# Performance work log

Measured on AMD Instinct MI355X. Metric: run time of the kernel, lower is better.

The kernel has to match this reference:

```python
import jax, jax.numpy as jnp
import numpy as np

N = 100000      # nodes
E = 1600000     # edges (before self-loops)
IN = 128        # in_channels
H = 8           # heads (layer 0)
C = 8           # hidden_node_channels_per_head
OUT = 64        # out_channels (layer 1, single head, concat=False)
NEG_SLOPE = 0.2 # PyG GATConv LeakyReLU slope


def setup_inputs() -> dict:
    key = jax.random.key(0)
    ks = jax.random.split(key, 10)
    x = jax.random.normal(ks[0], (N, IN), jnp.float32)
    edge_index = jax.random.randint(ks[1], (2, E), 0, N, dtype=jnp.int32)
    s0 = 1.0 / np.sqrt(IN)
    s1 = 1.0 / np.sqrt(H * C)
    return {
        "x": x,
        "edge_index": edge_index,
        "W0": jax.random.normal(ks[2], (IN, H * C), jnp.float32) * s0,
        "att_src0": jax.random.normal(ks[3], (H, C), jnp.float32) * s1,
        "att_dst0": jax.random.normal(ks[4], (H, C), jnp.float32) * s1,
        "b0": jnp.zeros((H * C,), jnp.float32),
        "W1": jax.random.normal(ks[5], (H * C, OUT), jnp.float32) * s1,
        "att_src1": jax.random.normal(ks[6], (1, OUT), jnp.float32) * s1,
        "att_dst1": jax.random.normal(ks[7], (1, OUT), jnp.float32) * s1,
        "b1": jnp.zeros((OUT,), jnp.float32),
    }


def _gat_conv(x, src, dst, W, a_src, a_dst, b, heads, ch, concat):
    # x: [N, F_in]; src/dst: [E'] (self-loops included)
    xW = (x @ W).reshape(N, heads, ch)                     # [N, H, C]
    a_s = jnp.einsum('nhc,hc->nh', xW, a_src)              # [N, H]
    a_d = jnp.einsum('nhc,hc->nh', xW, a_dst)              # [N, H]
    e = jax.nn.leaky_relu(a_s[src] + a_d[dst], NEG_SLOPE)  # [E', H]
    # segment softmax over incoming edges of each dst node
    m = jax.ops.segment_max(e, dst, num_segments=N)        # [N, H]
    ex = jnp.exp(e - m[dst])
    denom = jax.ops.segment_sum(ex, dst, num_segments=N)   # [N, H]
    alpha = ex / denom[dst]                                # [E', H]
    out = jax.ops.segment_sum(alpha[:, :, None] * xW[src], dst, num_segments=N)  # [N, H, C]
    if concat:
        return out.reshape(N, heads * ch) + b
    return out.mean(axis=1) + b


def reference(x, edge_index, W0, att_src0, att_dst0, b0, W1, att_src1, att_dst1, b1):
    src, dst = edge_index[0], edge_index[1]
    loops = jnp.arange(N, dtype=src.dtype)                 # PyG add_self_loops=True
    src = jnp.concatenate([src, loops])
    dst = jnp.concatenate([dst, loops])
    # layer 0: GATConv(IN -> C per head, H heads, concat) ; ELU (dropout = identity at eval)
    h = jax.nn.elu(_gat_conv(x, src, dst, W0, att_src0, att_dst0, b0, H, C, True))
    # layer 1: GATConv(H*C -> OUT, 1 head, concat=False) ; ELU
    out = jax.nn.elu(_gat_conv(h, src, dst, W1, att_src1, att_dst1, b1, 1, OUT, False))
    return out
```

## Files before the change

kernel.cpp:

```cpp
#include <hip/hip_runtime.h>
#include <hip/hip_fp16.h>
#include <math.h>


#define CAPS 16
#define STRIDE 17
#define NBMAX 512
#define LOG2E 1.44269504f

typedef _Float16 h2_t  __attribute__((ext_vector_type(2)));
typedef _Float16 h8_t  __attribute__((ext_vector_type(8)));
typedef float    f4_t  __attribute__((ext_vector_type(4)));
typedef unsigned int u4_t __attribute__((ext_vector_type(4)));

__device__ __forceinline__ float lrelu(float v) { return v >= 0.f ? v : 0.2f * v; }
__device__ __forceinline__ float eluf(float v)  {
    return v > 0.f ? v : __builtin_amdgcn_exp2f(v * LOG2E) - 1.f;
}

#define MIX_LO(acc, pk, w) asm("v_fma_mix_f32 %0, %1, %2, %0 op_sel:[0,0,0] op_sel_hi:[1,0,0]" : "+v"(acc) : "v"(pk), "v"(w))
#define MIX_HI(acc, pk, w) asm("v_fma_mix_f32 %0, %1, %2, %0 op_sel:[1,0,0] op_sel_hi:[1,0,0]" : "+v"(acc) : "v"(pk), "v"(w))

__device__ __forceinline__ void gemm_body(
    int gb, const float* __restrict__ x, int N,
    __half* __restrict__ xw, float* __restrict__ as, float* __restrict__ ad,
    h8_t* Bl)
{
    int wave = threadIdx.x >> 6, lane = threadIdx.x & 63;
    int row0 = gb * 128 + wave * 16;
    if (row0 >= N) return;
    int quad = lane >> 4, c16 = lane & 15;
    int myrow = min(row0 + c16, N - 1);
    const float* xr = x + (size_t)myrow * 128;
    h8_t a[4];
    #pragma unroll
    for (int ks = 0; ks < 4; ks++) {
        int kb = ks * 32 + quad * 8;
        float4 v0 = *(const float4*)(xr + kb);
        float4 v1 = *(const float4*)(xr + kb + 4);
        h8_t av;
        av[0] = (_Float16)v0.x; av[1] = (_Float16)v0.y;
        av[2] = (_Float16)v0.z; av[3] = (_Float16)v0.w;
        av[4] = (_Float16)v1.x; av[5] = (_Float16)v1.y;
        av[6] = (_Float16)v1.z; av[7] = (_Float16)v1.w;
        a[ks] = av;
    }
    int rbase = row0 + quad * 4;
    #pragma unroll
    for (int ct = 0; ct < 5; ct++) {
        f4_t acc = {0.f, 0.f, 0.f, 0.f};
        #pragma unroll
        for (int ks = 0; ks < 4; ks++) {
            h8_t b = Bl[(ct * 4 + ks) * 64 + lane];
            acc = __builtin_amdgcn_mfma_f32_16x16x32_f16(a[ks], b, acc, 0, 0, 0);
        }
        if (ct < 4) {
            int col = ct * 16 + c16;
            #pragma unroll
            for (int r = 0; r < 4; r++) {
                int row = rbase + r;
                if (row < N) xw[(size_t)row * 64 + col] = __float2half(acc[r]);
            }
        } else {
            #pragma unroll
            for (int r = 0; r < 4; r++) {
                int row = rbase + r;
                if (row < N) {
                    float sc = acc[r] * LOG2E;
                    if (c16 < 8) as[(size_t)row * 8 + c16] = sc;
                    else         ad[(size_t)row * 8 + (c16 - 8)] = sc;
                }
            }
        }
    }
}

__global__ __launch_bounds__(512, 4) void kGB(
    const float* __restrict__ x, const float* __restrict__ W0,
    const float* __restrict__ aS0, const float* __restrict__ aD0, int N,
    __half* __restrict__ xw, float* __restrict__ as, float* __restrict__ ad,
    int gemmBlocks,
    const int* __restrict__ src, const int* __restrict__ dst, int E, int perBlock,
    unsigned* __restrict__ bucketBuf, int* __restrict__ gcur, int NB, int cap,
    int binBlocks)
{
    __shared__ __align__(16) char smem[NBMAX * STRIDE * 4 + NBMAX * 4];
    int b = blockIdx.x;
    int T = gemmBlocks + binBlocks;
    int lo = (int)((long long)b * gemmBlocks / T);
    int hi = (int)((long long)(b + 1) * gemmBlocks / T);
    if (hi > lo) {
        h8_t* Bl = (h8_t*)smem;
        for (int g = threadIdx.x; g < 1280; g += 512) {
            int col  = g & 15;
            int quad = (g >> 4) & 3;
            int ks   = (g >> 6) & 3;
            int ct   = g >> 8;
            h8_t av;
            if (ct < 4) {
                #pragma unroll
                for (int j = 0; j < 8; j++) {
                    int k = ks * 32 + quad * 8 + j;
                    av[j] = (_Float16)W0[k * 64 + ct * 16 + col];
                }
            } else {
                int h = col & 7;
                const float* att = (col < 8) ? aS0 : aD0;
                #pragma unroll
                for (int j = 0; j < 8; j++) {
                    int k = ks * 32 + quad * 8 + j;
                    float v = 0.f;
                    #pragma unroll
                    for (int cc = 0; cc < 8; cc++)
                        v += W0[k * 64 + h * 8 + cc] * att[h * 8 + cc];
                    av[j] = (_Float16)v;
                }
            }
            Bl[g] = av;
        }
        __syncthreads();
        gemm_body(lo, x, N, xw, as, ad, Bl);
    } else {
        int pb = b - hi;
        unsigned* stage = (unsigned*)smem;
        int* scnt = (int*)(smem + NBMAX * STRIDE * 4);
        int tid = threadIdx.x;
        for (int i = tid; i < NB; i += 512) scnt[i] = 0;
        __syncthreads();
        int e0 = pb * perBlock, e1 = min(E, e0 + perBlock);
        for (int i = e0 + tid; i < e1; i += 512) {
            int d2 = dst[i], s2 = src[i];
            int bk = d2 >> 8;
            unsigned rec = ((unsigned)(d2 & 255) << 22) | (unsigned)s2;
            int pos = atomicAdd(&scnt[bk], 1);
            if (pos < CAPS) {
                stage[bk * STRIDE + pos] = rec;
            } else {
                int g = atomicAdd(&gcur[bk], 1);
                if (g < cap) bucketBuf[(size_t)bk * cap + g] = rec;
            }
        }
        __syncthreads();
        for (int t = tid; t < NB; t += 512) {
            int n = min(scnt[t], CAPS);
            if (n > 0) {
                int gb2 = atomicAdd(&gcur[t], n);
                unsigned* gp = &bucketBuf[(size_t)t * cap + gb2];
                for (int j = 0; j < n; j++)
                    if (gb2 + j < cap) gp[j] = stage[t * STRIDE + j];
            }
        }
    }
}

__global__ __launch_bounds__(256) void kP2(
    const unsigned* __restrict__ bucketBuf, const int* __restrict__ gcur,
    int NB, int cap, int N, int* __restrict__ row, int* __restrict__ adj)
{
    __shared__ int deg[256];
    __shared__ int curl[256];
    __shared__ int sc[256];
    int b = blockIdx.x, tid = threadIdx.x;
    int lo = b << 8;
    int hi = min(N, lo + 256);
    int cnt = hi - lo;
    int size = min(gcur[b], cap);
    int part = 0;
    for (int i = tid; i < b; i += 256) part += min(gcur[i], cap);
    sc[tid] = part;
    __syncthreads();
    for (int off = 128; off > 0; off >>= 1) {
        if (tid < off) sc[tid] += sc[tid + off];
        __syncthreads();
    }
    int bbase = sc[0];
    __syncthreads();
    deg[tid] = 0;
    __syncthreads();
    const unsigned* buf = bucketBuf + (size_t)b * cap;
    for (int e = tid; e < size; e += 256) atomicAdd(&deg[buf[e] >> 22], 1);
    __syncthreads();
    int d = deg[tid];
    sc[tid] = d;
    __syncthreads();
    for (int off = 1; off < 256; off <<= 1) {
        int xv = (tid >= off) ? sc[tid - off] : 0;
        __syncthreads();
        sc[tid] += xv;
        __syncthreads();
    }
    int o = (tid ? sc[tid - 1] : 0);
    curl[tid] = o;
    if (tid < cnt) row[lo + tid] = bbase + o;
    if (b == NB - 1 && tid == 0) row[N] = bbase + size;
    __syncthreads();
    for (int e = tid; e < size; e += 256) {
        unsigned r = buf[e];
        int l = r >> 22;
        int p = atomicAdd(&curl[l], 1);
        adj[bbase + p] = (int)(r & 0x3FFFFF);
    }
}

__global__ __launch_bounds__(512) void k_agg8(
    const __half* __restrict__ xw, const float* __restrict__ as, const float* __restrict__ ad,
    const int* __restrict__ row, const int* __restrict__ adj,
    const float* __restrict__ bias, int N, __half* __restrict__ hbuf)
{
    int n = (blockIdx.x * 512 + threadIdx.x) >> 4;
    int sub  = threadIdx.x & 15;
    if (n >= N) return;
    int e2 = sub >> 3;
    int hh = sub & 7;
    int rs = row[n], re = row[n + 1];
    const u4_t* xwv = (const u4_t*)xw;
    float adv = ad[(unsigned)n * 8u + hh];
    float shift = lrelu(as[(unsigned)n * 8u + hh] + adv);
    float accv[8];
    #pragma unroll
    for (int k = 0; k < 8; k++) accv[k] = 0.f;
    float dsum = 0.f;

    int j = rs;
    bool vA0 = j + e2 < re,     vB0 = j + 2 + e2 < re;
    int  sA0 = adj[(unsigned)(vA0 ? j + e2 : 0)];
    int  sB0 = adj[(unsigned)(vB0 ? j + 2 + e2 : 0)];
    bool vA1 = j + 4 + e2 < re, vB1 = j + 6 + e2 < re;
    int  sA1 = adj[(unsigned)(vA1 ? j + 4 + e2 : 0)];
    int  sB1 = adj[(unsigned)(vB1 ? j + 6 + e2 : 0)];
    float eA0 = lrelu(as[(unsigned)sA0 * 8u + hh] + adv);
    float eB0 = lrelu(as[(unsigned)sB0 * 8u + hh] + adv);
    u4_t xA0 = xwv[(unsigned)sA0 * 8u + hh];
    u4_t xB0 = xwv[(unsigned)sB0 * 8u + hh];
    float eA1, eB1; u4_t xA1, xB1;

    for (;;) {
        {
            bool vA2 = j + 8 + e2 < re, vB2 = j + 10 + e2 < re;
            int nsA = adj[(unsigned)(vA2 ? j + 8 + e2 : 0)];
            int nsB = adj[(unsigned)(vB2 ? j + 10 + e2 : 0)];
            eA1 = lrelu(as[(unsigned)sA1 * 8u + hh] + adv);
            eB1 = lrelu(as[(unsigned)sB1 * 8u + hh] + adv);
            xA1 = xwv[(unsigned)sA1 * 8u + hh];
            xB1 = xwv[(unsigned)sB1 * 8u + hh];
            float wA = vA0 ? __builtin_amdgcn_exp2f(eA0 - shift) : 0.f;
            float wB = vB0 ? __builtin_amdgcn_exp2f(eB0 - shift) : 0.f;
            dsum += wA + wB;
            #pragma unroll
            for (int q = 0; q < 4; q++) {
                MIX_LO(accv[2 * q],     xA0[q], wA);
                MIX_HI(accv[2 * q + 1], xA0[q], wA);
            }
            #pragma unroll
            for (int q = 0; q < 4; q++) {
                MIX_LO(accv[2 * q],     xB0[q], wB);
                MIX_HI(accv[2 * q + 1], xB0[q], wB);
            }
            vA0 = vA2; vB0 = vB2; sA0 = nsA; sB0 = nsB;
        }
        j += 4;
        if (!__any(vA1)) break;
        {
            bool vA2 = j + 8 + e2 < re, vB2 = j + 10 + e2 < re;
            int nsA = adj[(unsigned)(vA2 ? j + 8 + e2 : 0)];
            int nsB = adj[(unsigned)(vB2 ? j + 10 + e2 : 0)];
            eA0 = lrelu(as[(unsigned)sA0 * 8u + hh] + adv);
            eB0 = lrelu(as[(unsigned)sB0 * 8u + hh] + adv);
            xA0 = xwv[(unsigned)sA0 * 8u + hh];
            xB0 = xwv[(unsigned)sB0 * 8u + hh];
            float wA = vA1 ? __builtin_amdgcn_exp2f(eA1 - shift) : 0.f;
            float wB = vB1 ? __builtin_amdgcn_exp2f(eB1 - shift) : 0.f;
            dsum += wA + wB;
            #pragma unroll
            for (int q = 0; q < 4; q++) {
                MIX_LO(accv[2 * q],     xA1[q], wA);
                MIX_HI(accv[2 * q + 1], xA1[q], wA);
            }
            #pragma unroll
            for (int q = 0; q < 4; q++) {
                MIX_LO(accv[2 * q],     xB1[q], wB);
                MIX_HI(accv[2 * q + 1], xB1[q], wB);
            }
            vA1 = vA2; vB1 = vB2; sA1 = nsA; sB1 = nsB;
        }
        j += 4;
        if (!__any(vA0)) break;
    }
    #pragma unroll
    for (int k = 0; k < 8; k++) accv[k] += __shfl_xor(accv[k], 8, 64);
    dsum += __shfl_xor(dsum, 8, 64);
    if (e2 == 0) {
        float inv = 1.f / (1.f + dsum);
        h8_t sv = *(const h8_t*)(xw + (size_t)n * 64 + hh * 8);
        float4 b0 = *(const float4*)(bias + hh * 8);
        float4 b1 = *(const float4*)(bias + hh * 8 + 4);
        float bb[8] = {b0.x, b0.y, b0.z, b0.w, b1.x, b1.y, b1.z, b1.w};
        h8_t o;
        #pragma unroll
        for (int k = 0; k < 8; k++) {
            float v = (accv[k] + (float)sv[k]) * inv + bb[k];
            o[k] = (_Float16)eluf(v);
        }
        *(h8_t*)(hbuf + (size_t)n * 64 + hh * 8) = o;
    }
}

__global__ __launch_bounds__(512, 4) void kTF1(
    const __half* __restrict__ h, const float* __restrict__ W1,
    const float* __restrict__ aS1, const float* __restrict__ aD1, int N,
    __half* __restrict__ hw, float* __restrict__ as1, float* __restrict__ ad1)
{
    __shared__ __align__(16) h8_t Bl[512];
    {
        int g = threadIdx.x;
        int col  = g & 15;
        int quad = (g >> 4) & 3;
        int ks   = (g >> 6) & 1;
        int ct   = g >> 7;
        h8_t av;
        #pragma unroll
        for (int j = 0; j < 8; j++) {
            int k = ks * 32 + quad * 8 + j;
            av[j] = (_Float16)W1[k * 64 + ct * 16 + col];
        }
        Bl[g] = av;
    }
    __syncthreads();
    int wave = threadIdx.x >> 6, lane = threadIdx.x & 63;
    int row0 = blockIdx.x * 128 + wave * 16;
    if (row0 >= N) return;
    int quad = lane >> 4, c16 = lane & 15;
    int myrow = min(row0 + c16, N - 1);
    const __half* hr = h + (size_t)myrow * 64;
    h8_t a0 = *(const h8_t*)(hr + quad * 8);
    h8_t a1 = *(const h8_t*)(hr + 32 + quad * 8);
    int rbase = row0 + quad * 4;
    float ps[4] = {0.f, 0.f, 0.f, 0.f};
    float pd[4] = {0.f, 0.f, 0.f, 0.f};
    #pragma unroll
    for (int ct = 0; ct < 4; ct++) {
        f4_t acc = {0.f, 0.f, 0.f, 0.f};
        acc = __builtin_amdgcn_mfma_f32_16x16x32_f16(a0, Bl[(ct * 2 + 0) * 64 + lane], acc, 0, 0, 0);
        acc = __builtin_amdgcn_mfma_f32_16x16x32_f16(a1, Bl[(ct * 2 + 1) * 64 + lane], acc, 0, 0, 0);
        float s1c = aS1[ct * 16 + c16];
        float d1c = aD1[ct * 16 + c16];
        int col = ct * 16 + c16;
        #pragma unroll
        for (int r = 0; r < 4; r++) {
            int rr = rbase + r;
            if (rr < N) hw[(size_t)rr * 64 + col] = __float2half(acc[r]);
            ps[r] = fmaf(acc[r], s1c, ps[r]);
            pd[r] = fmaf(acc[r], d1c, pd[r]);
        }
    }
    #pragma unroll
    for (int r = 0; r < 4; r++) {
        #pragma unroll
        for (int off = 1; off < 16; off <<= 1) {
            ps[r] += __shfl_xor(ps[r], off, 64);
            pd[r] += __shfl_xor(pd[r], off, 64);
        }
    }
    if (c16 == 0) {
        #pragma unroll
        for (int r = 0; r < 4; r++) {
            int rr = rbase + r;
            if (rr < N) { as1[rr] = ps[r] * LOG2E; ad1[rr] = pd[r] * LOG2E; }
        }
    }
}

__global__ __launch_bounds__(512) void k_agg1(
    const __half* __restrict__ hw, const float* __restrict__ as, const float* __restrict__ ad,
    const int* __restrict__ row, const int* __restrict__ adj,
    const float* __restrict__ bias, int N, float* __restrict__ outp)
{
    int n = (blockIdx.x * 512 + threadIdx.x) >> 4;
    int sub  = threadIdx.x & 15;
    if (n >= N) return;
    int e2 = sub >> 3;
    int hh = sub & 7;
    int rs = row[n], re = row[n + 1];
    const u4_t* hwv = (const u4_t*)hw;
    float adv = ad[n];
    float shift = lrelu(as[n] + adv);
    float accv[8];
    #pragma unroll
    for (int k = 0; k < 8; k++) accv[k] = 0.f;
    float dsum = 0.f;

    int j = rs;
    bool vA0 = j + e2 < re,     vB0 = j + 2 + e2 < re;
    int  sA0 = adj[(unsigned)(vA0 ? j + e2 : 0)];
    int  sB0 = adj[(unsigned)(vB0 ? j + 2 + e2 : 0)];
    bool vA1 = j + 4 + e2 < re, vB1 = j + 6 + e2 < re;
    int  sA1 = adj[(unsigned)(vA1 ? j + 4 + e2 : 0)];
    int  sB1 = adj[(unsigned)(vB1 ? j + 6 + e2 : 0)];
    float eA0 = lrelu(as[(unsigned)sA0] + adv);
    float eB0 = lrelu(as[(unsigned)sB0] + adv);
    u4_t xA0 = hwv[(unsigned)sA0 * 8u + hh];
    u4_t xB0 = hwv[(unsigned)sB0 * 8u + hh];
    float eA1, eB1; u4_t xA1, xB1;

    for (;;) {
        {
            bool vA2 = j + 8 + e2 < re, vB2 = j + 10 + e2 < re;
            int nsA = adj[(unsigned)(vA2 ? j + 8 + e2 : 0)];
            int nsB = adj[(unsigned)(vB2 ? j + 10 + e2 : 0)];
            eA1 = lrelu(as[(unsigned)sA1] + adv);
            eB1 = lrelu(as[(unsigned)sB1] + adv);
            xA1 = hwv[(unsigned)sA1 * 8u + hh];
            xB1 = hwv[(unsigned)sB1 * 8u + hh];
            float wA = vA0 ? __builtin_amdgcn_exp2f(eA0 - shift) : 0.f;
            float wB = vB0 ? __builtin_amdgcn_exp2f(eB0 - shift) : 0.f;
            dsum += wA + wB;
            #pragma unroll
            for (int q = 0; q < 4; q++) {
                MIX_LO(accv[2 * q],     xA0[q], wA);
                MIX_HI(accv[2 * q + 1], xA0[q], wA);
            }
            #pragma unroll
            for (int q = 0; q < 4; q++) {
                MIX_LO(accv[2 * q],     xB0[q], wB);
                MIX_HI(accv[2 * q + 1], xB0[q], wB);
            }
            vA0 = vA2; vB0 = vB2; sA0 = nsA; sB0 = nsB;
        }
        j += 4;
        if (!__any(vA1)) break;
        {
            bool vA2 = j + 8 + e2 < re, vB2 = j + 10 + e2 < re;
            int nsA = adj[(unsigned)(vA2 ? j + 8 + e2 : 0)];
            int nsB = adj[(unsigned)(vB2 ? j + 10 + e2 : 0)];
            eA0 = lrelu(as[(unsigned)sA0] + adv);
            eB0 = lrelu(as[(unsigned)sB0] + adv);
            xA0 = hwv[(unsigned)sA0 * 8u + hh];
            xB0 = hwv[(unsigned)sB0 * 8u + hh];
            float wA = vA1 ? __builtin_amdgcn_exp2f(eA1 - shift) : 0.f;
            float wB = vB1 ? __builtin_amdgcn_exp2f(eB1 - shift) : 0.f;
            dsum += wA + wB;
            #pragma unroll
            for (int q = 0; q < 4; q++) {
                MIX_LO(accv[2 * q],     xA1[q], wA);
                MIX_HI(accv[2 * q + 1], xA1[q], wA);
            }
            #pragma unroll
            for (int q = 0; q < 4; q++) {
                MIX_LO(accv[2 * q],     xB1[q], wB);
                MIX_HI(accv[2 * q + 1], xB1[q], wB);
            }
            vA1 = vA2; vB1 = vB2; sA1 = nsA; sB1 = nsB;
        }
        j += 4;
        if (!__any(vA0)) break;
    }
    #pragma unroll
    for (int k = 0; k < 8; k++) accv[k] += __shfl_xor(accv[k], 8, 64);
    dsum += __shfl_xor(dsum, 8, 64);
    if (e2 == 0) {
        float inv = 1.f / (1.f + dsum);
        h8_t sv = *(const h8_t*)(hw + (size_t)n * 64 + hh * 8);
        float4 b0 = *(const float4*)(bias + hh * 8);
        float4 b1 = *(const float4*)(bias + hh * 8 + 4);
        float bb[8] = {b0.x, b0.y, b0.z, b0.w, b1.x, b1.y, b1.z, b1.w};
        float ov[8];
        #pragma unroll
        for (int k = 0; k < 8; k++)
            ov[k] = eluf((accv[k] + (float)sv[k]) * inv + bb[k]);
        float4 o0 = {ov[0], ov[1], ov[2], ov[3]};
        float4 o1 = {ov[4], ov[5], ov[6], ov[7]};
        float4* op = (float4*)(outp + (size_t)n * 64 + hh * 8);
        op[0] = o0;
        op[1] = o1;
    }
}

extern "C" void kernel_launch(void* const* d_in, const int* in_sizes, int n_in,
                              void* d_out, int out_size, void* d_ws, size_t ws_size,
                              hipStream_t stream)
{
    const float* x   = (const float*)d_in[0];
    const int*   ei  = (const int*)d_in[1];
    const float* W0  = (const float*)d_in[2];
    const float* aS0 = (const float*)d_in[3];
    const float* aD0 = (const float*)d_in[4];
    const float* b0  = (const float*)d_in[5];
    const float* W1  = (const float*)d_in[6];
    const float* aS1 = (const float*)d_in[7];
    const float* aD1 = (const float*)d_in[8];
    const float* b1  = (const float*)d_in[9];

    const int N = in_sizes[0] / 128;
    const int E = in_sizes[1] / 2;
    const int* srcp = ei;
    const int* dstp = ei + E;

    const int NB  = (N + 255) >> 8;
    const int cap = E / NB + 4096;

    char* ws = (char*)d_ws;
    size_t off = 0;
    auto alloc = [&](size_t bytes) -> size_t {
        size_t o = off;
        off = (o + bytes + 255) & ~(size_t)255;
        return o;
    };
    __half* B1 = (__half*)(ws + alloc((size_t)N * 64 * 2));
    size_t b2Bytes = (size_t)N * 64 * 2;
    size_t bkBytes = (size_t)NB * cap * 4;
    char*  region  = ws + alloc(b2Bytes > bkBytes ? b2Bytes : bkBytes);
    __half*   B2        = (__half*)region;
    unsigned* bucketBuf = (unsigned*)region;
    float* as0 = (float*)(ws + alloc((size_t)N * 8 * 4));
    float* ad0 = (float*)(ws + alloc((size_t)N * 8 * 4));
    float* as1 = (float*)(ws + alloc((size_t)N * 4));
    float* ad1 = (float*)(ws + alloc((size_t)N * 4));
    int*   row = (int*)(ws + alloc((size_t)(N + 1) * 4));
    int*   adj = (int*)(ws + alloc((size_t)E * 4));
    int*  gcur = (int*)(ws + alloc((size_t)NB * 4));

    const int gemmBlocks = (N + 127) / 128;
    const int binBlocks  = 512;
    const int perBlock   = (E + binBlocks - 1) / binBlocks;

    hipMemsetAsync(gcur, 0, (size_t)NB * 4, stream);
    kGB<<<gemmBlocks + binBlocks, 512, 0, stream>>>(
        x, W0, aS0, aD0, N, B1, as0, ad0, gemmBlocks,
        srcp, dstp, E, perBlock, bucketBuf, gcur, NB, cap, binBlocks);
    kP2<<<NB, 256, 0, stream>>>(bucketBuf, gcur, NB, cap, N, row, adj);

    const int agBlocks = (N + 31) / 32;
    k_agg8<<<agBlocks, 512, 0, stream>>>(B1, as0, ad0, row, adj, b0, N, B2);
    kTF1<<<(N + 127) / 128, 512, 0, stream>>>(B2, W1, aS1, aD1, N, B1, as1, ad1);
    k_agg1<<<agBlocks, 512, 0, stream>>>(B1, as1, ad1, row, adj, b1, N, (float*)d_out);
}
```

Before: 244.6 us.

## Fuse layer-1 feature transform into layer-0 aggregation kernel via shared memory

Folds the layer-1 MFMA transform (h @ W1 plus the attention projections) into the layer-0 aggregation kernel. Each block stages its 32 output rows of h in LDS and two waves run the MFMA, so the intermediate h never makes a round trip through global memory and one launch is removed. The costs are a __syncthreads per block, a reload of W1 into LDS in every one of roughly 3125 blocks, and six of eight waves idling during the transform. Out-of-range threads now stay alive to reach the barrier instead of returning early.

```diff
diff --git a/kernel.cpp b/kernel.cpp
--- a/kernel.cpp
+++ b/kernel.cpp
@@ -205,17 +205,37 @@
 __global__ __launch_bounds__(512) void k_agg8(
     const __half* __restrict__ xw, const float* __restrict__ as, const float* __restrict__ ad,
     const int* __restrict__ row, const int* __restrict__ adj,
-    const float* __restrict__ bias, int N, __half* __restrict__ hbuf)
+    const float* __restrict__ bias,
+    const float* __restrict__ W1, const float* __restrict__ aS1, const float* __restrict__ aD1,
+    int N, __half* __restrict__ hw, float* __restrict__ as1, float* __restrict__ ad1)
 {
+    __shared__ __align__(16) h8_t Wl[512];
+    __shared__ __align__(16) h8_t hst[32][9];
+    {
+        int g = threadIdx.x;
+        int col  = g & 15;
+        int quad = (g >> 4) & 3;
+        int ks   = (g >> 6) & 1;
+        int ct   = g >> 7;
+        h8_t av;
+        #pragma unroll
+        for (int j = 0; j < 8; j++) {
+            int k = ks * 32 + quad * 8 + j;
+            av[j] = (_Float16)W1[k * 64 + ct * 16 + col];
+        }
+        Wl[g] = av;
+    }
     int n = (blockIdx.x * 512 + threadIdx.x) >> 4;
     int sub  = threadIdx.x & 15;
-    if (n >= N) return;
+    bool active = n < N;
     int e2 = sub >> 3;
     int hh = sub & 7;
-    int rs = row[n], re = row[n + 1];
+    int rs = active ? row[n] : 0;
+    int re = active ? row[n + 1] : 0;
     const u4_t* xwv = (const u4_t*)xw;
-    float adv = ad[(unsigned)n * 8u + hh];
-    float shift = lrelu(as[(unsigned)n * 8u + hh] + adv);
+    unsigned nc = active ? (unsigned)n : 0u;
+    float adv = ad[nc * 8u + hh];
+    float shift = lrelu(as[nc * 8u + hh] + adv);
     float accv[8];
     #pragma unroll
     for (int k = 0; k < 8; k++) accv[k] = 0.f;
@@ -290,82 +310,66 @@
     for (int k = 0; k < 8; k++) accv[k] += __shfl_xor(accv[k], 8, 64);
     dsum += __shfl_xor(dsum, 8, 64);
     if (e2 == 0) {
-        float inv = 1.f / (1.f + dsum);
-        h8_t sv = *(const h8_t*)(xw + (size_t)n * 64 + hh * 8);
-        float4 b0 = *(const float4*)(bias + hh * 8);
-        float4 b1 = *(const float4*)(bias + hh * 8 + 4);
-        float bb[8] = {b0.x, b0.y, b0.z, b0.w, b1.x, b1.y, b1.z, b1.w};
+        int nl = (threadIdx.x >> 4);
         h8_t o;
+        if (active) {
+            float inv = 1.f / (1.f + dsum);
+            h8_t sv = *(const h8_t*)(xw + (size_t)n * 64 + hh * 8);
+            float4 b0 = *(const float4*)(bias + hh * 8);
+            float4 b1 = *(const float4*)(bias + hh * 8 + 4);
+            float bb[8] = {b0.x, b0.y, b0.z, b0.w, b1.x, b1.y, b1.z, b1.w};
+            #pragma unroll
+            for (int k = 0; k < 8; k++) {
+                float v = (accv[k] + (float)sv[k]) * inv + bb[k];
+                o[k] = (_Float16)eluf(v);
+            }
+        } else {
+            #pragma unroll
+            for (int k = 0; k < 8; k++) o[k] = (_Float16)0.f;
+        }
+        hst[nl][hh] = o;
+    }
+    __syncthreads();
+    int wave = threadIdx.x >> 6, lane = threadIdx.x & 63;
+    if (wave < 2) {
+        int quad = lane >> 4, c16 = lane & 15;
+        int lrow = wave * 16 + c16;
+        int row0 = blockIdx.x * 32 + wave * 16;
+        h8_t a0 = hst[lrow][quad];
+        h8_t a1 = hst[lrow][4 + quad];
+        int rbase = row0 + quad * 4;
+        float ps[4] = {0.f, 0.f, 0.f, 0.f};
+        float pd[4] = {0.f, 0.f, 0.f, 0.f};
         #pragma unroll
-        for (int k = 0; k < 8; k++) {
-            float v = (accv[k] + (float)sv[k]) * inv + bb[k];
-            o[k] = (_Float16)eluf(v);
-        }
-        *(h8_t*)(hbuf + (size_t)n * 64 + hh * 8) = o;
-    }
-}
-
-__global__ __launch_bounds__(512, 4) void kTF1(
-    const __half* __restrict__ h, const float* __restrict__ W1,
-    const float* __restrict__ aS1, const float* __restrict__ aD1, int N,
-    __half* __restrict__ hw, float* __restrict__ as1, float* __restrict__ ad1)
-{
-    __shared__ __align__(16) h8_t Bl[512];
-    {
-        int g = threadIdx.x;
-        int col  = g & 15;
-        int quad = (g >> 4) & 3;
-        int ks   = (g >> 6) & 1;
-        int ct   = g >> 7;
-        h8_t av;
-        #pragma unroll
-        for (int j = 0; j < 8; j++) {
-            int k = ks * 32 + quad * 8 + j;
-            av[j] = (_Float16)W1[k * 64 + ct * 16 + col];
-        }
-        Bl[g] = av;
-    }
-    __syncthreads();
-    int wave = threadIdx.x >> 6, lane = threadIdx.x & 63;
-    int row0 = blockIdx.x * 128 + wave * 16;
-    if (row0 >= N) return;
-    int quad = lane >> 4, c16 = lane & 15;
-    int myrow = min(row0 + c16, N - 1);
-    const __half* hr = h + (size_t)myrow * 64;
-    h8_t a0 = *(const h8_t*)(hr + quad * 8);
-    h8_t a1 = *(const h8_t*)(hr + 32 + quad * 8);
-    int rbase = row0 + quad * 4;
-    float ps[4] = {0.f, 0.f, 0.f, 0.f};
-    float pd[4] = {0.f, 0.f, 0.f, 0.f};
-    #pragma unroll
-    for (int ct = 0; ct < 4; ct++) {
-        f4_t acc = {0.f, 0.f, 0.f, 0.f};
-        acc = __builtin_amdgcn_mfma_f32_16x16x32_f16(a0, Bl[(ct * 2 + 0) * 64 + lane], acc, 0, 0, 0);
-        acc = __builtin_amdgcn_mfma_f32_16x16x32_f16(a1, Bl[(ct * 2 + 1) * 64 + lane], acc, 0, 0, 0);
-        float s1c = aS1[ct * 16 + c16];
-        float d1c = aD1[ct * 16 + c16];
-        int col = ct * 16 + c16;
+        for (int ct = 0; ct < 4; ct++) {
+            f4_t acc = {0.f, 0.f, 0.f, 0.f};
+            acc = __builtin_amdgcn_mfma_f32_16x16x32_f16(a0, Wl[(ct * 2 + 0) * 64 + lane], acc, 0, 0, 0);
+            acc = __builtin_amdgcn_mfma_f32_16x16x32_f16(a1, Wl[(ct * 2 + 1) * 64 + lane], acc, 0, 0, 0);
+            float s1c = aS1[ct * 16 + c16];
+            float d1c = aD1[ct * 16 + c16];
+            int col = ct * 16 + c16;
+            #pragma unroll
+            for (int r = 0; r < 4; r++) {
+                int rr = rbase + r;
+                if (rr < N) hw[(size_t)rr * 64 + col] = __float2half(acc[r]);
+                ps[r] = fmaf(acc[r], s1c, ps[r]);
+                pd[r] = fmaf(acc[r], d1c, pd[r]);
+            }
+        }
         #pragma unroll
         for (int r = 0; r < 4; r++) {
-            int rr = rbase + r;
-            if (rr < N) hw[(size_t)rr * 64 + col] = __float2half(acc[r]);
-            ps[r] = fmaf(acc[r], s1c, ps[r]);
-            pd[r] = fmaf(acc[r], d1c, pd[r]);
-        }
-    }
-    #pragma unroll
-    for (int r = 0; r < 4; r++) {
-        #pragma unroll
-        for (int off = 1; off < 16; off <<= 1) {
-            ps[r] += __shfl_xor(ps[r], off, 64);
-            pd[r] += __shfl_xor(pd[r], off, 64);
-        }
-    }
-    if (c16 == 0) {
-        #pragma unroll
-        for (int r = 0; r < 4; r++) {
-            int rr = rbase + r;
-            if (rr < N) { as1[rr] = ps[r] * LOG2E; ad1[rr] = pd[r] * LOG2E; }
+            #pragma unroll
+            for (int off = 1; off < 16; off <<= 1) {
+                ps[r] += __shfl_xor(ps[r], off, 64);
+                pd[r] += __shfl_xor(pd[r], off, 64);
+            }
+        }
+        if (c16 == 0) {
+            #pragma unroll
+            for (int r = 0; r < 4; r++) {
+                int rr = rbase + r;
+                if (rr < N) { as1[rr] = ps[r] * LOG2E; ad1[rr] = pd[r] * LOG2E; }
+            }
         }
     }
 }
@@ -530,7 +534,7 @@
     kP2<<<NB, 256, 0, stream>>>(bucketBuf, gcur, NB, cap, N, row, adj);
 
     const int agBlocks = (N + 31) / 32;
-    k_agg8<<<agBlocks, 512, 0, stream>>>(B1, as0, ad0, row, adj, b0, N, B2);
-    kTF1<<<(N + 127) / 128, 512, 0, stream>>>(B2, W1, aS1, aD1, N, B1, as1, ad1);
-    k_agg1<<<agBlocks, 512, 0, stream>>>(B1, as1, ad1, row, adj, b1, N, (float*)d_out);
-}
+    k_agg8<<<agBlocks, 512, 0, stream>>>(B1, as0, ad0, row, adj, b0,
+                                         W1, aS1, aD1, N, B2, as1, ad1);
+    k_agg1<<<agBlocks, 512, 0, stream>>>(B2, as1, ad1, row, adj, b1, N, (float*)d_out);
+}
```

After: 238.3 us. 2.6% less time.
